# Kernel tuning notes

Measured on AMD Instinct MI355X. Metric: run time of the kernel, lower is better.

The kernel has to match this reference:

```python
import jax, jax.numpy as jnp
import numpy as np


def _lstm_last(x, w_ih, w_hh, b_ih, b_hh):
    # x: [M, T, D] -> last hidden state [M, H]; PyTorch gate order i,f,g,o
    M = x.shape[0]
    H = w_hh.shape[1]
    xi = jnp.einsum('mtd,gd->tmg', x, w_ih) + b_ih + b_hh  # [T, M, 4H]
    def step(carry, xt):
        h, c = carry
        gates = xt + h @ w_hh.T
        i, f, g, o = jnp.split(gates, 4, axis=-1)
        c = jax.nn.sigmoid(f) * c + jax.nn.sigmoid(i) * jnp.tanh(g)
        h = jax.nn.sigmoid(o) * jnp.tanh(c)
        return (h, c), None
    z = jnp.zeros((M, H), x.dtype)
    (h, _), _ = jax.lax.scan(step, (z, z), xi)
    return h


def _gcn_conv(x, edge_index, w, b):
    # Symmetric-normalized GCN conv with self loops (PyG GCNConv defaults).
    # x: [BT, N, F] -> [BT, N, Hg]
    N = x.shape[1]
    loops = jnp.arange(N, dtype=edge_index.dtype)
    src = jnp.concatenate([edge_index[0], loops])
    dst = jnp.concatenate([edge_index[1], loops])
    deg = jnp.zeros((N,), x.dtype).at[dst].add(jnp.ones((), x.dtype))
    dinv = jax.lax.rsqrt(deg)  # deg >= 1 thanks to self loops
    norm = (dinv[src] * dinv[dst])[:, None]  # [E+N, 1]
    xw = x @ w                               # [BT, N, Hg]
    msg = xw[:, src, :] * norm               # gather along node axis
    out = jnp.zeros_like(xw).at[:, dst, :].add(msg)  # scatter-add
    return out + b


def setup_inputs() -> dict:
    key = jax.random.key(0)
    ks = jax.random.split(key, 16)
    B, T, N, F = 2, 12, 10000, 16
    Hg, H, P, E = 32, 64, 4, 160000
    sc = 0.1
    return {
        'era5_seq': jax.random.normal(ks[0], (B, T, N, F), jnp.float32),
        'zeta_seq': jax.random.normal(ks[1], (B, T, N), jnp.float32),
        'edge_index': jax.random.randint(ks[2], (2, E), 0, N, jnp.int32),
        'gcn_w': jax.random.normal(ks[3], (F, Hg), jnp.float32) * sc,
        'gcn_b': jnp.zeros((Hg,), jnp.float32),
        'w_ih1': jax.random.normal(ks[4], (4 * H, Hg), jnp.float32) * sc,
        'w_hh1': jax.random.normal(ks[5], (4 * H, H), jnp.float32) * sc,
        'b_ih1': jax.random.normal(ks[6], (4 * H,), jnp.float32) * sc,
        'b_hh1': jax.random.normal(ks[7], (4 * H,), jnp.float32) * sc,
        'w_ih2': jax.random.normal(ks[8], (4 * H, 1), jnp.float32) * sc,
        'w_hh2': jax.random.normal(ks[9], (4 * H, H), jnp.float32) * sc,
        'b_ih2': jax.random.normal(ks[10], (4 * H,), jnp.float32) * sc,
        'b_hh2': jax.random.normal(ks[11], (4 * H,), jnp.float32) * sc,
        'fc_w': jax.random.normal(ks[12], (P, 2 * H), jnp.float32) * sc,
        'fc_b': jnp.zeros((P,), jnp.float32),
    }


def reference(era5_seq, zeta_seq, edge_index, gcn_w, gcn_b, w_ih1, w_hh1, b_ih1, b_hh1, w_ih2, w_hh2, b_ih2, b_hh2, fc_w, fc_b):
    B, T, N, F = era5_seq.shape
    Hg = gcn_w.shape[1]
    # GCN over all (b, t) slices at once (replaces nested python loops)
    h = _gcn_conv(era5_seq.reshape(B * T, N, F), edge_index, gcn_w, gcn_b)
    gcn_seq = h.reshape(B, T, N, Hg).transpose(0, 2, 1, 3).reshape(B * N, T, Hg)
    spatial_feat = _lstm_last(gcn_seq, w_ih1, w_hh1, b_ih1, b_hh1)  # [B*N, H]
    z_seq = zeta_seq.transpose(0, 2, 1).reshape(B * N, T, 1)
    zeta_feat = _lstm_last(z_seq, w_ih2, w_hh2, b_ih2, b_hh2)        # [B*N, H]
    combined = jnp.concatenate([spatial_feat, zeta_feat], axis=-1)
    y = combined @ fc_w.T + fc_b                                     # [B*N, P]
    return y.reshape(B, N, -1).transpose(0, 2, 1)                    # [B, P, N]
```

## Files before the change

### kernel.cpp

```cpp
#include <hip/hip_runtime.h>
#include <hip/hip_bf16.h>
#include <stdint.h>

#define NN 10000
#define EE 160000
#define BB 2
#define TT 12
#define FF 16
#define HG 32
#define HH 64
#define PP 4
#define BT (BB*TT)
#define MM (BB*NN)
#define CAP 96
#define L2E 1.4426950408889634f

typedef _Float16 half8 __attribute__((ext_vector_type(8)));
typedef _Float16 h2 __attribute__((ext_vector_type(2)));
typedef float f32x4 __attribute__((ext_vector_type(4)));

union UP { uint32_t u; h2 h; };

__device__ __forceinline__ float sigm2(float a) {
  return __builtin_amdgcn_rcpf(1.0f + __builtin_amdgcn_exp2f(-a));
}
__device__ __forceinline__ float tanh2(float a) {
  return fmaf(-2.0f, __builtin_amdgcn_rcpf(1.0f + __builtin_amdgcn_exp2f(a)), 1.0f);
}

#define FILL_BLKS (EE / 256)
#define NT ((NN + 255) / 256)
#define PREP_BLKS (NT * TT)
__global__ __launch_bounds__(256) void k_prepfill(
    const int* __restrict__ eidx, int* __restrict__ cnt, int* __restrict__ csr,
    const float* __restrict__ era5, uint4* __restrict__ xt) {
  const int bid = blockIdx.x;
  if (bid < FILL_BLKS) {
    int e = bid * 256 + threadIdx.x;
    int d = eidx[EE + e];
    int pos = atomicAdd(&cnt[d], 1);
    if (pos < CAP) csr[d * CAP + pos] = eidx[e];
    return;
  }
  const int p = bid - FILL_BLKS;
  const int btp = p % TT;
  const int n = (p / TT) * 256 + threadIdx.x;
  if (n >= NN) return;
  const f32x4* r0 = (const f32x4*)(era5 + ((size_t)(2 * btp) * NN + n) * FF);
  const f32x4* r1 = (const f32x4*)(era5 + ((size_t)(2 * btp + 1) * NN + n) * FF);
  uint32_t o[8];
#pragma unroll
  for (int q = 0; q < 4; ++q) {
    f32x4 v = r0[q];
    UP a, b;
    a.h[0] = (_Float16)v[0]; a.h[1] = (_Float16)v[1];
    b.h[0] = (_Float16)v[2]; b.h[1] = (_Float16)v[3];
    o[2 * q] = a.u; o[2 * q + 1] = b.u;
  }
  uint4* dst = xt + (size_t)n * 48 + btp * 4;
  dst[0] = make_uint4(o[0], o[1], o[2], o[3]);
  dst[1] = make_uint4(o[4], o[5], o[6], o[7]);
#pragma unroll
  for (int q = 0; q < 4; ++q) {
    f32x4 v = r1[q];
    UP a, b;
    a.h[0] = (_Float16)v[0]; a.h[1] = (_Float16)v[1];
    b.h[0] = (_Float16)v[2]; b.h[1] = (_Float16)v[3];
    o[2 * q] = a.u; o[2 * q + 1] = b.u;
  }
  dst[2] = make_uint4(o[0], o[1], o[2], o[3]);
  dst[3] = make_uint4(o[4], o[5], o[6], o[7]);
}

__global__ __launch_bounds__(256) void k_gather(const uint32_t* __restrict__ xt,
                                                const int* __restrict__ csr,
                                                const int* __restrict__ cnt,
                                                const float* __restrict__ gw,
                                                const float* __restrict__ gb,
                                                uint32_t* __restrict__ gout) {
  __shared__ float wsm[FF * HG];
  __shared__ float gbs[HG];
  __shared__ float agg[4][BT][FF];
  const int tid = threadIdx.x;
  wsm[tid] = gw[tid];
  wsm[tid + 256] = gw[tid + 256];
  if (tid < HG) gbs[tid] = gb[tid];

  const int dloc = tid >> 6, lane = tid & 63;
  const int dst = blockIdx.x * 4 + dloc;
  const int cdst = min(cnt[dst], CAP);
  const float dinv_d = rsqrtf((float)cdst + 1.0f);

  float acc[6];
#pragma unroll
  for (int i = 0; i < 6; ++i) acc[i] = 0.f;

  for (int base = 0; base < cdst; base += 64) {
    int mine = base + lane;
    int sv = dst; float dvv = 0.f;
    if (mine < cdst) {
      sv = csr[dst * CAP + mine];
      dvv = rsqrtf((float)cnt[sv] + 1.0f);
    }
    const int lim = min(64, cdst - base);
    for (int j = 0; j < lim; j += 8) {
      int sj[8]; float dj[8];
#pragma unroll
      for (int u = 0; u < 8; ++u) {
        int idx = j + u;
        sj[u] = __shfl(sv, idx);
        float d = __shfl(dvv, idx);
        dj[u] = (idx < lim) ? d : 0.f;
      }
      uint32_t dw[8][3];
#pragma unroll
      for (int u = 0; u < 8; ++u) {
        const uint32_t* row = xt + (size_t)sj[u] * 192;
#pragma unroll
        for (int k = 0; k < 3; ++k) dw[u][k] = row[lane + 64 * k];
      }
#pragma unroll
      for (int u = 0; u < 8; ++u) {
#pragma unroll
        for (int k = 0; k < 3; ++k) {
          UP up; up.u = dw[u][k];
          acc[2 * k]     = fmaf((float)up.h[0], dj[u], acc[2 * k]);
          acc[2 * k + 1] = fmaf((float)up.h[1], dj[u], acc[2 * k + 1]);
        }
      }
    }
  }
  const uint32_t* srow = xt + (size_t)dst * 192;
#pragma unroll
  for (int k = 0; k < 3; ++k) {
    UP u; u.u = srow[lane + 64 * k];
    int d0 = lane + 64 * k;
    int bt = d0 >> 3, f = (d0 & 7) * 2;
    agg[dloc][bt][f]     = (acc[2 * k]     + (float)u.h[0] * dinv_d) * dinv_d;
    agg[dloc][bt][f + 1] = (acc[2 * k + 1] + (float)u.h[1] * dinv_d) * dinv_d;
  }
  __syncthreads();
#pragma unroll
  for (int k = 0; k < 3; ++k) {
    int d0 = lane + 64 * k;
    int t = d0 >> 4, c0 = (d0 & 15) * 2;
#pragma unroll
    for (int b = 0; b < 2; ++b) {
      const float* av = agg[dloc][b * TT + t];
      float v0 = gbs[c0], v1 = gbs[c0 + 1];
#pragma unroll
      for (int f = 0; f < FF; ++f) {
        v0 = fmaf(av[f], wsm[f * HG + c0], v0);
        v1 = fmaf(av[f], wsm[f * HG + c0 + 1], v1);
      }
      UP u; u.h[0] = (_Float16)v0; u.h[1] = (_Float16)v1;
      gout[((size_t)(b * NN + dst)) * 192 + d0] = u.u;
    }
  }
}

__global__ __launch_bounds__(256) void k_lstmfc(
    const _Float16* __restrict__ gout, const float* __restrict__ zeta,
    const float* __restrict__ w_ih1, const float* __restrict__ w_hh1,
    const float* __restrict__ b_ih1, const float* __restrict__ b_hh1,
    const float* __restrict__ w_ih2, const float* __restrict__ w_hh2,
    const float* __restrict__ b_ih2, const float* __restrict__ b_hh2,
    const float* __restrict__ fc_w, const float* __restrict__ fc_b,
    float* __restrict__ out) {
  const int m0 = blockIdx.x * 16;
  const int b = (m0 >= NN) ? 1 : 0;
  const int n0 = m0 - b * NN;
  const int tid = threadIdx.x;
  const int wave = tid >> 6;
  const int lane = tid & 63;
  const int col = lane & 15;
  const int quad = lane >> 4;

  half8 Bx[4];
  half8 Bh1[4][2];
  half8 Bh2[4][2];
  float bias1[4], bias2[4], wx[4];
#pragma unroll
  for (int g = 0; g < 4; ++g) {
    const float sc = (g == 2) ? 2.0f * L2E : L2E;
    int ncol = 16 * (wave + 4 * g) + col;
    bias1[g] = (b_ih1[ncol] + b_hh1[ncol]) * sc;
    bias2[g] = (b_ih2[ncol] + b_hh2[ncol]) * sc;
    wx[g] = w_ih2[ncol] * sc;
#pragma unroll
    for (int j = 0; j < 8; ++j)
      Bx[g][j] = (_Float16)(w_ih1[ncol * HG + quad * 8 + j] * sc);
#pragma unroll
    for (int c2 = 0; c2 < 2; ++c2) {
#pragma unroll
      for (int j = 0; j < 8; ++j) {
        Bh1[g][c2][j] = (_Float16)(w_hh1[ncol * HH + c2 * 32 + quad * 8 + j] * sc);
        Bh2[g][c2][j] = (_Float16)(w_hh2[ncol * HH + c2 * 32 + quad * 8 + j] * sc);
      }
    }
  }

  __shared__ float zbuf[TT][16];
  if (tid < TT * 16) {
    int t = tid >> 4, s = tid & 15;
    zbuf[t][s] = zeta[((size_t)b * TT + t) * NN + n0 + s];
  }
  __shared__ __align__(16) _Float16 hb1[2][16 * 72];
  __shared__ __align__(16) _Float16 hb2[2][16 * 72];
  __shared__ float fcb[16][132];

  const _Float16* gbase = gout + (size_t)(m0 + col) * (TT * HG) + quad * 8;
  half8 A0 = *(const half8*)(gbase);

  float c1[4] = {0.f, 0.f, 0.f, 0.f}, c2v[4] = {0.f, 0.f, 0.f, 0.f};
  float h1f[4], h2f[4];

  __syncthreads();

#pragma unroll
  for (int t = 0; t < TT; ++t) {
    const int p = t & 1;
    if (t > 0) {
#pragma unroll
      for (int r = 0; r < 4; ++r) {
        int a = (quad * 4 + r) * 72 + 16 * wave + col;
        hb1[p][a] = (_Float16)h1f[r];
        hb2[p][a] = (_Float16)h2f[r];
      }
    }
    f32x4 a1[4], a2[4];
#pragma unroll
    for (int g = 0; g < 4; ++g) {
      f32x4 ai; ai[0] = bias1[g]; ai[1] = bias1[g]; ai[2] = bias1[g]; ai[3] = bias1[g];
      a1[g] = __builtin_amdgcn_mfma_f32_16x16x32_f16(A0, Bx[g], ai, 0, 0, 0);
#pragma unroll
      for (int r = 0; r < 4; ++r)
        a2[g][r] = fmaf(wx[g], zbuf[t][quad * 4 + r], bias2[g]);
    }
    if (t < TT - 1) A0 = *(const half8*)(gbase + (t + 1) * HG);
    if (t > 0) {
      __syncthreads();
      const half8 A11 = *(const half8*)(&hb1[p][col * 72 + quad * 8]);
      const half8 A21 = *(const half8*)(&hb1[p][col * 72 + 32 + quad * 8]);
      const half8 A12 = *(const half8*)(&hb2[p][col * 72 + quad * 8]);
      const half8 A22 = *(const half8*)(&hb2[p][col * 72 + 32 + quad * 8]);
#pragma unroll
      for (int g = 0; g < 4; ++g) {
        a1[g] = __builtin_amdgcn_mfma_f32_16x16x32_f16(A11, Bh1[g][0], a1[g], 0, 0, 0);
        a1[g] = __builtin_amdgcn_mfma_f32_16x16x32_f16(A21, Bh1[g][1], a1[g], 0, 0, 0);
        a2[g] = __builtin_amdgcn_mfma_f32_16x16x32_f16(A12, Bh2[g][0], a2[g], 0, 0, 0);
        a2[g] = __builtin_amdgcn_mfma_f32_16x16x32_f16(A22, Bh2[g][1], a2[g], 0, 0, 0);
      }
    }
#pragma unroll
    for (int r = 0; r < 4; ++r) {
      float i1 = sigm2(a1[0][r]), f1 = sigm2(a1[1][r]);
      float g1 = tanh2(a1[2][r]), o1 = sigm2(a1[3][r]);
      c1[r] = fmaf(f1, c1[r], i1 * g1);
      h1f[r] = o1 * tanh2(c1[r] * (2.0f * L2E));
      float i2 = sigm2(a2[0][r]), f2 = sigm2(a2[1][r]);
      float g2 = tanh2(a2[2][r]), o2 = sigm2(a2[3][r]);
      c2v[r] = fmaf(f2, c2v[r], i2 * g2);
      h2f[r] = o2 * tanh2(c2v[r] * (2.0f * L2E));
    }
  }
#pragma unroll
  for (int r = 0; r < 4; ++r) {
    fcb[quad * 4 + r][16 * wave + col] = h1f[r];
    fcb[quad * 4 + r][64 + 16 * wave + col] = h2f[r];
  }
  __syncthreads();
  if (tid < 64) {
    int pp = tid >> 4, s = tid & 15;
    const f32x4* wr = (const f32x4*)(fc_w + pp * 128);
    const float* hv = fcb[s];
    float acc = fc_b[pp];
#pragma unroll
    for (int k = 0; k < 32; ++k) {
      f32x4 w4 = wr[k];
      acc += w4[0] * hv[4 * k] + w4[1] * hv[4 * k + 1] +
             w4[2] * hv[4 * k + 2] + w4[3] * hv[4 * k + 3];
    }
    out[((size_t)(b * PP + pp)) * NN + n0 + s] = acc;
  }
}

extern "C" void kernel_launch(void* const* d_in, const int* in_sizes, int n_in,
                              void* d_out, int out_size, void* d_ws, size_t ws_size,
                              hipStream_t stream) {
  (void)in_sizes; (void)n_in; (void)out_size; (void)ws_size;
  const float* era5  = (const float*)d_in[0];
  const float* zeta  = (const float*)d_in[1];
  const int*   eidx  = (const int*)d_in[2];
  const float* gcn_w = (const float*)d_in[3];
  const float* gcn_b = (const float*)d_in[4];
  const float* w_ih1 = (const float*)d_in[5];
  const float* w_hh1 = (const float*)d_in[6];
  const float* b_ih1 = (const float*)d_in[7];
  const float* b_hh1 = (const float*)d_in[8];
  const float* w_ih2 = (const float*)d_in[9];
  const float* w_hh2 = (const float*)d_in[10];
  const float* b_ih2 = (const float*)d_in[11];
  const float* b_hh2 = (const float*)d_in[12];
  const float* fc_w  = (const float*)d_in[13];
  const float* fc_b  = (const float*)d_in[14];
  float* out = (float*)d_out;

  char* ws = (char*)d_ws;
  int*      cnt  = (int*)(ws);
  int*      csr  = (int*)(ws + (64 << 10));
  uint32_t* xt   = (uint32_t*)(ws + (4ull << 20));
  _Float16* gout = (_Float16*)(ws + (12ull << 20));

  hipMemsetAsync(cnt, 0, NN * sizeof(int), stream);
  k_prepfill<<<FILL_BLKS + PREP_BLKS, 256, 0, stream>>>(eidx, cnt, csr, era5,
                                                        (uint4*)xt);
  k_gather<<<NN / 4, 256, 0, stream>>>(xt, csr, cnt, gcn_w, gcn_b, (uint32_t*)gout);
  k_lstmfc<<<MM / 16, 256, 0, stream>>>(gout, zeta, w_ih1, w_hh1, b_ih1, b_hh1,
                                        w_ih2, w_hh2, b_ih2, b_hh2, fc_w, fc_b, out);
}
```

Before: 184.3 us.

## Process two 16-row tiles per LSTM block to amortize weight loads and barriers

Each LSTM/FC block now handles 32 sequences (two independent 16-row tiles) instead of 16, halving the grid. Register-resident recurrent weights and per-step barriers are shared across both tiles, and the two independent MFMA chains can interleave to hide latency. In exchange register pressure rises (doubled accumulators and state), which may reduce occupancy, and there are half as many blocks to spread across CUs.

Result: slower. 202.1 us (+9.7%).

```diff
diff --git a/kernel.cpp b/kernel.cpp
--- a/kernel.cpp
+++ b/kernel.cpp
@@ -167,9 +167,11 @@
     const float* __restrict__ b_ih2, const float* __restrict__ b_hh2,
     const float* __restrict__ fc_w, const float* __restrict__ fc_b,
     float* __restrict__ out) {
-  const int m0 = blockIdx.x * 16;
-  const int b = (m0 >= NN) ? 1 : 0;
-  const int n0 = m0 - b * NN;
+  const int base_m = blockIdx.x * 32;
+  const int bA = (base_m >= NN) ? 1 : 0;
+  const int n0A = base_m - bA * NN;
+  const int bB = (base_m + 16 >= NN) ? 1 : 0;
+  const int n0B = base_m + 16 - bB * NN;
   const int tid = threadIdx.x;
   const int wave = tid >> 6;
   const int lane = tid & 63;
@@ -200,20 +202,29 @@
     }
   }
 
-  __shared__ float zbuf[TT][16];
-  if (tid < TT * 16) {
-    int t = tid >> 4, s = tid & 15;
-    zbuf[t][s] = zeta[((size_t)b * TT + t) * NN + n0 + s];
-  }
-  __shared__ __align__(16) _Float16 hb1[2][16 * 72];
-  __shared__ __align__(16) _Float16 hb2[2][16 * 72];
+  __shared__ float zbuf[2][TT][16];
+  for (int i = tid; i < 2 * TT * 16; i += 256) {
+    int tl = i / (TT * 16);
+    int rem = i - tl * (TT * 16);
+    int t = rem >> 4, s = rem & 15;
+    int bb = tl ? bB : bA;
+    int nn = tl ? n0B : n0A;
+    zbuf[tl][t][s] = zeta[((size_t)bb * TT + t) * NN + nn + s];
+  }
+  __shared__ __align__(16) _Float16 hb1[2][2][16 * 72];
+  __shared__ __align__(16) _Float16 hb2[2][2][16 * 72];
   __shared__ float fcb[16][132];
 
-  const _Float16* gbase = gout + (size_t)(m0 + col) * (TT * HG) + quad * 8;
-  half8 A0 = *(const half8*)(gbase);
-
-  float c1[4] = {0.f, 0.f, 0.f, 0.f}, c2v[4] = {0.f, 0.f, 0.f, 0.f};
-  float h1f[4], h2f[4];
+  const _Float16* gbaseA = gout + (size_t)(base_m + col) * (TT * HG) + quad * 8;
+  const _Float16* gbaseB = gout + (size_t)(base_m + 16 + col) * (TT * HG) + quad * 8;
+  half8 A0a = *(const half8*)(gbaseA);
+  half8 A0b = *(const half8*)(gbaseB);
+
+  float c1[2][4], c2v[2][4], h1f[2][4], h2f[2][4];
+#pragma unroll
+  for (int tl = 0; tl < 2; ++tl)
+#pragma unroll
+    for (int r = 0; r < 4; ++r) { c1[tl][r] = 0.f; c2v[tl][r] = 0.f; }
 
   __syncthreads();
 
@@ -222,66 +233,85 @@
     const int p = t & 1;
     if (t > 0) {
 #pragma unroll
-      for (int r = 0; r < 4; ++r) {
-        int a = (quad * 4 + r) * 72 + 16 * wave + col;
-        hb1[p][a] = (_Float16)h1f[r];
-        hb2[p][a] = (_Float16)h2f[r];
-      }
-    }
-    f32x4 a1[4], a2[4];
+      for (int tl = 0; tl < 2; ++tl)
+#pragma unroll
+        for (int r = 0; r < 4; ++r) {
+          int a = (quad * 4 + r) * 72 + 16 * wave + col;
+          hb1[p][tl][a] = (_Float16)h1f[tl][r];
+          hb2[p][tl][a] = (_Float16)h2f[tl][r];
+        }
+    }
+    f32x4 a1[2][4], a2[2][4];
 #pragma unroll
     for (int g = 0; g < 4; ++g) {
       f32x4 ai; ai[0] = bias1[g]; ai[1] = bias1[g]; ai[2] = bias1[g]; ai[3] = bias1[g];
-      a1[g] = __builtin_amdgcn_mfma_f32_16x16x32_f16(A0, Bx[g], ai, 0, 0, 0);
-#pragma unroll
-      for (int r = 0; r < 4; ++r)
-        a2[g][r] = fmaf(wx[g], zbuf[t][quad * 4 + r], bias2[g]);
-    }
-    if (t < TT - 1) A0 = *(const half8*)(gbase + (t + 1) * HG);
+      a1[0][g] = __builtin_amdgcn_mfma_f32_16x16x32_f16(A0a, Bx[g], ai, 0, 0, 0);
+      a1[1][g] = __builtin_amdgcn_mfma_f32_16x16x32_f16(A0b, Bx[g], ai, 0, 0, 0);
+#pragma unroll
+      for (int r = 0; r < 4; ++r) {
+        a2[0][g][r] = fmaf(wx[g], zbuf[0][t][quad * 4 + r], bias2[g]);
+        a2[1][g][r] = fmaf(wx[g], zbuf[1][t][quad * 4 + r], bias2[g]);
+      }
+    }
+    if (t < TT - 1) {
+      A0a = *(const half8*)(gbaseA + (t + 1) * HG);
+      A0b = *(const half8*)(gbaseB + (t + 1) * HG);
+    }
     if (t > 0) {
       __syncthreads();
-      const half8 A11 = *(const half8*)(&hb1[p][col * 72 + quad * 8]);
-      const half8 A21 = *(const half8*)(&hb1[p][col * 72 + 32 + quad * 8]);
-      const half8 A12 = *(const half8*)(&hb2[p][col * 72 + quad * 8]);
-      const half8 A22 = *(const half8*)(&hb2[p][col * 72 + 32 + quad * 8]);
-#pragma unroll
-      for (int g = 0; g < 4; ++g) {
-        a1[g] = __builtin_amdgcn_mfma_f32_16x16x32_f16(A11, Bh1[g][0], a1[g], 0, 0, 0);
-        a1[g] = __builtin_amdgcn_mfma_f32_16x16x32_f16(A21, Bh1[g][1], a1[g], 0, 0, 0);
-        a2[g] = __builtin_amdgcn_mfma_f32_16x16x32_f16(A12, Bh2[g][0], a2[g], 0, 0, 0);
-        a2[g] = __builtin_amdgcn_mfma_f32_16x16x32_f16(A22, Bh2[g][1], a2[g], 0, 0, 0);
-      }
-    }
+#pragma unroll
+      for (int tl = 0; tl < 2; ++tl) {
+        const half8 A11 = *(const half8*)(&hb1[p][tl][col * 72 + quad * 8]);
+        const half8 A21 = *(const half8*)(&hb1[p][tl][col * 72 + 32 + quad * 8]);
+        const half8 A12 = *(const half8*)(&hb2[p][tl][col * 72 + quad * 8]);
+        const half8 A22 = *(const half8*)(&hb2[p][tl][col * 72 + 32 + quad * 8]);
+#pragma unroll
+        for (int g = 0; g < 4; ++g) {
+          a1[tl][g] = __builtin_amdgcn_mfma_f32_16x16x32_f16(A11, Bh1[g][0], a1[tl][g], 0, 0, 0);
+          a1[tl][g] = __builtin_amdgcn_mfma_f32_16x16x32_f16(A21, Bh1[g][1], a1[tl][g], 0, 0, 0);
+          a2[tl][g] = __builtin_amdgcn_mfma_f32_16x16x32_f16(A12, Bh2[g][0], a2[tl][g], 0, 0, 0);
+          a2[tl][g] = __builtin_amdgcn_mfma_f32_16x16x32_f16(A22, Bh2[g][1], a2[tl][g], 0, 0, 0);
+        }
+      }
+    }
+#pragma unroll
+    for (int tl = 0; tl < 2; ++tl)
+#pragma unroll
+      for (int r = 0; r < 4; ++r) {
+        float i1 = sigm2(a1[tl][0][r]), f1 = sigm2(a1[tl][1][r]);
+        float g1 = tanh2(a1[tl][2][r]), o1 = sigm2(a1[tl][3][r]);
+        c1[tl][r] = fmaf(f1, c1[tl][r], i1 * g1);
+        h1f[tl][r] = o1 * tanh2(c1[tl][r] * (2.0f * L2E));
+        float i2 = sigm2(a2[tl][0][r]), f2 = sigm2(a2[tl][1][r]);
+        float g2 = tanh2(a2[tl][2][r]), o2 = sigm2(a2[tl][3][r]);
+        c2v[tl][r] = fmaf(f2, c2v[tl][r], i2 * g2);
+        h2f[tl][r] = o2 * tanh2(c2v[tl][r] * (2.0f * L2E));
+      }
+  }
+#pragma unroll
+  for (int tl = 0; tl < 2; ++tl) {
+    __syncthreads();
 #pragma unroll
     for (int r = 0; r < 4; ++r) {
-      float i1 = sigm2(a1[0][r]), f1 = sigm2(a1[1][r]);
-      float g1 = tanh2(a1[2][r]), o1 = sigm2(a1[3][r]);
-      c1[r] = fmaf(f1, c1[r], i1 * g1);
-      h1f[r] = o1 * tanh2(c1[r] * (2.0f * L2E));
-      float i2 = sigm2(a2[0][r]), f2 = sigm2(a2[1][r]);
-      float g2 = tanh2(a2[2][r]), o2 = sigm2(a2[3][r]);
-      c2v[r] = fmaf(f2, c2v[r], i2 * g2);
-      h2f[r] = o2 * tanh2(c2v[r] * (2.0f * L2E));
-    }
-  }
-#pragma unroll
-  for (int r = 0; r < 4; ++r) {
-    fcb[quad * 4 + r][16 * wave + col] = h1f[r];
-    fcb[quad * 4 + r][64 + 16 * wave + col] = h2f[r];
-  }
-  __syncthreads();
-  if (tid < 64) {
-    int pp = tid >> 4, s = tid & 15;
-    const f32x4* wr = (const f32x4*)(fc_w + pp * 128);
-    const float* hv = fcb[s];
-    float acc = fc_b[pp];
-#pragma unroll
-    for (int k = 0; k < 32; ++k) {
-      f32x4 w4 = wr[k];
-      acc += w4[0] * hv[4 * k] + w4[1] * hv[4 * k + 1] +
-             w4[2] * hv[4 * k + 2] + w4[3] * hv[4 * k + 3];
-    }
-    out[((size_t)(b * PP + pp)) * NN + n0 + s] = acc;
+      fcb[quad * 4 + r][16 * wave + col] = h1f[tl][r];
+      fcb[quad * 4 + r][64 + 16 * wave + col] = h2f[tl][r];
+    }
+    __syncthreads();
+    if (tid < 64) {
+      int pp = tid >> 4, s = tid & 15;
+      const f32x4* wr = (const f32x4*)(fc_w + pp * 128);
+      const float* hv = fcb[s];
+      float acc = fc_b[pp];
+#pragma unroll
+      for (int k = 0; k < 32; ++k) {
+        f32x4 w4 = wr[k];
+        acc += w4[0] * hv[4 * k] + w4[1] * hv[4 * k + 1] +
+               w4[2] * hv[4 * k + 2] + w4[3] * hv[4 * k + 3];
+      }
+      int bb = tl ? bB : bA;
+      int nn = tl ? n0B : n0A;
+      out[((size_t)(bb * PP + pp)) * NN + nn + s] = acc;
+    }
   }
 }
 
@@ -316,6 +346,6 @@
   k_prepfill<<<FILL_BLKS + PREP_BLKS, 256, 0, stream>>>(eidx, cnt, csr, era5,
                                                         (uint4*)xt);
   k_gather<<<NN / 4, 256, 0, stream>>>(xt, csr, cnt, gcn_w, gcn_b, (uint32_t*)gout);
-  k_lstmfc<<<MM / 16, 256, 0, stream>>>(gout, zeta, w_ih1, w_hh1, b_ih1, b_hh1,
+  k_lstmfc<<<MM / 32, 256, 0, stream>>>(gout, zeta, w_ih1, w_hh1, b_ih1, b_hh1,
                                         w_ih2, w_hh2, b_ih2, b_hh2, fc_w, fc_b, out);
 }
```
